# Kernel optimization log

Measured on AMD Instinct MI355X. Metric: run time of the kernel, lower is better.

Reference implementation:

```python
import jax, jax.numpy as jnp
import numpy as np

B, N, C = 8, 2_000_000, 16


def _per_batch_loss(x, t, num_classes):
    """x: [N] float values, t: [N] int labels.
    For each label group: loss = mean(group) - mode(group) (scipy mode,
    ties -> smallest value), scattered back to every position of that label.
    """
    n = x.shape[0]
    # Sort primarily by label, secondarily by value (lexsort: last key primary).
    order = jnp.lexsort((x, t))
    xs = x[order]
    ts = t[order]
    # Run-length encode equal (label, value) pairs to count value multiplicity.
    new_run = jnp.concatenate(
        [jnp.ones((1,), bool), (ts[1:] != ts[:-1]) | (xs[1:] != xs[:-1])])
    run_id = jnp.cumsum(new_run) - 1                      # [N]
    run_cnt = jax.ops.segment_sum(jnp.ones(n, xs.dtype), run_id,
                                  num_segments=n)[run_id]  # count per element
    # Mode per label = smallest value attaining the max multiplicity.
    grp_max = jax.ops.segment_max(run_cnt, ts, num_segments=num_classes)
    mode = jax.ops.segment_min(
        jnp.where(run_cnt == grp_max[ts], xs, jnp.inf), ts,
        num_segments=num_classes)                         # [C]
    ssum = jax.ops.segment_sum(xs, ts, num_segments=num_classes)
    scnt = jax.ops.segment_sum(jnp.ones(n, xs.dtype), ts,
                               num_segments=num_classes)
    mean = ssum / jnp.maximum(scnt, 1.0)
    per_label = jnp.where(scnt > 0, mean - mode, 0.0)     # [C]
    return per_label[t]                                    # scatter back, [N]


def setup_inputs() -> dict:
    key = jax.random.key(0)
    k1, k2 = jax.random.split(key)
    inputs = jax.random.normal(k1, (B, N), dtype=jnp.float32)
    targets = jax.random.randint(k2, (B, N), 0, C, dtype=jnp.int32)
    return {"inputs": inputs, "targets": targets, "num_classes": C}


def reference(inputs, targets, num_classes):
    per_pos = jax.vmap(lambda x, t: _per_batch_loss(x, t, num_classes))(
        inputs, targets)                                   # [B, N]
    return jnp.mean(per_pos)
```

## Files before the change

kernel.cpp:

```cpp
#include <hip/hip_runtime.h>
#include <stdint.h>

#define NUM_C 16
#define NUM_B 8
#define RANGES 64
#define NBKT (NUM_C * RANGES)
#define CHUNK_S 8192
#define TAB 4096
#define MODE_CAP 3072
#define MAX_NB 8

__device__ __forceinline__ unsigned hash_u32(unsigned h) {
    h ^= h >> 16; h *= 0x85ebca6bu;
    h ^= h >> 13; h *= 0xc2b2ae35u;
    h ^= h >> 16;
    return h;
}
__device__ __forceinline__ unsigned canon_key(float v) {
    unsigned k = __float_as_uint(v);
    return (k == 0x80000000u) ? 0u : k;
}
__device__ __forceinline__ unsigned bucket_of(unsigned key, int c) {
    return ((unsigned)c << 6) | (hash_u32(key) >> 26);
}

__global__ void __launch_bounds__(512)
sort_kernel(const float* __restrict__ x, const int* __restrict__ t,
            long long N, int bbase, int nchunk,
            unsigned* __restrict__ keysout, unsigned short* __restrict__ offs)
{
    __shared__ unsigned hist[NBKT];
    __shared__ unsigned lout[CHUNK_S];
    const int lb = blockIdx.x / nchunk;
    const int ch = blockIdx.x % nchunk;
    const int b  = bbase + lb;
    const long long base = (long long)ch * CHUNK_S;
    const int count = (int)((N - base < CHUNK_S) ? (N - base) : CHUNK_S);
    const float* xb = x + (size_t)b * N + base;
    const int*   tb = t + (size_t)b * N + base;
    const int tid = threadIdx.x;

    for (int i = tid; i < NBKT; i += 512) hist[i] = 0u;
    __syncthreads();

    unsigned keys[16], pk[16];
    const int n4 = count >> 2;
    #pragma unroll
    for (int r = 0; r < 4; ++r) {
        const int idx4 = tid + r * 512;
        if (idx4 < n4) {
            float4 v  = ((const float4*)xb)[idx4];
            int4   cc = ((const int4*)tb)[idx4];
            unsigned k0 = canon_key(v.x), b0 = bucket_of(k0, cc.x);
            unsigned k1 = canon_key(v.y), b1 = bucket_of(k1, cc.y);
            unsigned k2 = canon_key(v.z), b2 = bucket_of(k2, cc.z);
            unsigned k3 = canon_key(v.w), b3 = bucket_of(k3, cc.w);
            unsigned p0 = atomicAdd(&hist[b0], 1u);
            unsigned p1 = atomicAdd(&hist[b1], 1u);
            unsigned p2 = atomicAdd(&hist[b2], 1u);
            unsigned p3 = atomicAdd(&hist[b3], 1u);
            keys[r*4+0] = k0; pk[r*4+0] = (b0 << 13) | p0;
            keys[r*4+1] = k1; pk[r*4+1] = (b1 << 13) | p1;
            keys[r*4+2] = k2; pk[r*4+2] = (b2 << 13) | p2;
            keys[r*4+3] = k3; pk[r*4+3] = (b3 << 13) | p3;
        }
    }
    unsigned kex = 0u, pkx = 0u; int hex = 0;
    {
        const int remi = (n4 << 2) + tid;
        if (remi < count) {
            unsigned k = canon_key(xb[remi]);
            unsigned bk = bucket_of(k, tb[remi]);
            unsigned p = atomicAdd(&hist[bk], 1u);
            kex = k; pkx = (bk << 13) | p; hex = 1;
        }
    }
    __syncthreads();

    for (int st = 1; st < NBKT; st <<= 1) {
        const int k0 = tid, k1 = tid + 512;
        unsigned v0 = hist[k0] + ((k0 >= st) ? hist[k0 - st] : 0u);
        unsigned v1 = hist[k1] + ((k1 >= st) ? hist[k1 - st] : 0u);
        __syncthreads();
        hist[k0] = v0; hist[k1] = v1;
        __syncthreads();
    }

    #pragma unroll
    for (int r = 0; r < 4; ++r) {
        const int idx4 = tid + r * 512;
        if (idx4 < n4) {
            #pragma unroll
            for (int c2 = 0; c2 < 4; ++c2) {
                unsigned bk = pk[r*4+c2] >> 13, p = pk[r*4+c2] & 8191u;
                lout[(bk ? hist[bk - 1] : 0u) + p] = keys[r*4+c2];
            }
        }
    }
    if (hex) {
        unsigned bk = pkx >> 13, p = pkx & 8191u;
        lout[(bk ? hist[bk - 1] : 0u) + p] = kex;
    }
    __syncthreads();

    unsigned* kb = keysout + (size_t)lb * N + base;
    if (count == CHUNK_S) {
        #pragma unroll
        for (int r = 0; r < 4; ++r)
            ((uint4*)kb)[tid + r * 512] = ((const uint4*)lout)[tid + r * 512];
    } else {
        for (int i = tid; i < count; i += 512) kb[i] = lout[i];
    }
    unsigned short* orow = offs + ((size_t)lb * nchunk + ch) * 1025;
    orow[tid]       = (unsigned short)(tid ? hist[tid - 1] : 0u);
    orow[tid + 512] = (unsigned short)hist[tid + 511];
    if (tid == 0) orow[1024] = (unsigned short)hist[1023];
}

__global__ void __launch_bounds__(512)
mode_kernel(const unsigned* __restrict__ keysout,
            const unsigned short* __restrict__ offs,
            long long N, int nchunk, int bbase,
            unsigned long long* __restrict__ best,
            double* __restrict__ psum,
            unsigned* __restrict__ pcnt)
{
    __shared__ unsigned keyt[TAB];
    __shared__ unsigned cnt16[TAB / 2];
    __shared__ unsigned staging[MODE_CAP];
    __shared__ unsigned scnt;
    __shared__ unsigned long long redb[8];
    __shared__ double reds[8];

    const unsigned lb = blockIdx.x >> 10;
    const unsigned g  = blockIdx.x & 1023u;
    const unsigned c  = g >> 6;
    const unsigned b  = (unsigned)bbase + lb;
    const int tid = threadIdx.x;

    const uint4 z4 = make_uint4(0u, 0u, 0u, 0u);
    for (int i = tid; i < TAB / 4; i += 512) ((uint4*)keyt)[i] = z4;
    for (int i = tid; i < TAB / 8; i += 512) ((uint4*)cnt16)[i] = z4;
    if (tid == 0) scnt = 0u;
    __syncthreads();

    const unsigned* kb = keysout + (size_t)lb * N;
    const unsigned short* ob = offs + (size_t)lb * nchunk * 1025;

    double ls = 0.0;
    unsigned mo = 0xFFFFFFFFu;

    const int lane = tid & 63, wid = tid >> 6;
    const int sub = lane >> 4, j = lane & 15;
    for (int q = wid * 4 + sub; q < nchunk; q += 32) {
        unsigned s = 0u, len = 0u, pos = 0u;
        if (j == 0) {
            const unsigned short* orow = ob + (size_t)q * 1025;
            s = orow[g];
            len = (unsigned)orow[g + 1] - s;
            pos = atomicAdd(&scnt, len);
        }
        s   = __shfl(s,   sub << 4);
        len = __shfl(len, sub << 4);
        pos = __shfl(pos, sub << 4);
        const unsigned* src = kb + (size_t)q * CHUNK_S + s;
        for (unsigned jj = (unsigned)j; jj < len; jj += 16u) {
            unsigned key = src[jj];
            ls += (double)__uint_as_float(key);
            unsigned o = (key & 0x80000000u) ? ~key : (key | 0x80000000u);
            if (o < mo) mo = o;
            unsigned sp = pos + jj;
            if (sp < MODE_CAP) staging[sp] = o;
        }
    }
    __syncthreads();

    const unsigned n = (scnt < MODE_CAP) ? scnt : MODE_CAP;
    unsigned bc = 0u, bo = 0xFFFFFFFFu;
    for (unsigned base0 = 0; base0 < n; base0 += 2048u) {
        unsigned od[4], h[4], old[4];
        int nv = 0;
        #pragma unroll
        for (int k = 0; k < 4; ++k) {
            unsigned idx = base0 + (unsigned)tid + (unsigned)k * 512u;
            if (idx < n) {
                unsigned o = staging[idx];
                od[k] = o; h[k] = hash_u32(o) & (TAB - 1);
                nv = k + 1;
            }
        }
        #pragma unroll
        for (int k = 0; k < 4; ++k)
            if (k < nv) old[k] = atomicCAS(&keyt[h[k]], 0u, od[k]);
        #pragma unroll
        for (int k = 0; k < 4; ++k) {
            if (k >= nv) continue;
            unsigned o = old[k], hh = h[k];
            const unsigned oo = od[k];
            unsigned cnt = 1u;
            while (o != 0u) {
                if (o == oo) {
                    unsigned sh = (hh & 1u) << 4;
                    unsigned ret = atomicAdd(&cnt16[hh >> 1], 1u << sh);
                    cnt = ((ret >> sh) & 0xFFFFu) + 2u;
                    break;
                }
                hh = (hh + 1u) & (TAB - 1u);
                o = atomicCAS(&keyt[hh], 0u, oo);
            }
            if (cnt >= 2u && (cnt > bc || (cnt == bc && oo < bo))) {
                bc = cnt; bo = oo;
            }
        }
    }

    unsigned long long lbst = bc ? (((unsigned long long)bc << 32)
                                    | (unsigned long long)(~bo)) : 0ull;
    {
        unsigned long long s1 = (1ull << 32) | (unsigned long long)(~mo);
        if (s1 > lbst) lbst = s1;
    }
    #pragma unroll
    for (int sh = 32; sh > 0; sh >>= 1) {
        unsigned long long obv = __shfl_down(lbst, sh);
        if (obv > lbst) lbst = obv;
        ls += __shfl_down(ls, sh);
    }
    if ((tid & 63) == 0) { redb[wid] = lbst; reds[wid] = ls; }
    __syncthreads();
    if (tid == 0) {
        unsigned long long bb = 0ull; double ss = 0.0;
        #pragma unroll
        for (int i = 0; i < 8; ++i) {
            if (redb[i] > bb) bb = redb[i];
            ss += reds[i];
        }
        psum[b * NBKT + g] = ss;
        pcnt[b * NBKT + g] = scnt;
        if (bb) atomicMax(&best[b * NUM_C + c], bb);
    }
}

__global__ void __launch_bounds__(128)
finalize_kernel(const double* __restrict__ psum,
                const unsigned* __restrict__ pcnt,
                const unsigned long long* __restrict__ best,
                float* __restrict__ out, double inv_total)
{
    __shared__ double acc[NUM_B * NUM_C];
    const int i = threadIdx.x;
    const int b = i >> 4, c = i & 15;

    double s = 0.0;
    unsigned long long cnt = 0ull;
    const double*   ps = psum + (size_t)b * NBKT + ((size_t)c << 6);
    const unsigned* pc = pcnt + (size_t)b * NBKT + ((size_t)c << 6);
    for (int r = 0; r < 64; ++r) { s += ps[r]; cnt += pc[r]; }

    double term = 0.0;
    if (cnt > 0ull) {
        unsigned long long p = best[i];
        unsigned ord = 0xFFFFFFFFu - (unsigned)(p & 0xFFFFFFFFull);
        unsigned ub  = (ord & 0x80000000u) ? (ord ^ 0x80000000u) : ~ord;
        float mode = __uint_as_float(ub);
        term = s - (double)cnt * (double)mode;
    }
    acc[i] = term;
    __syncthreads();
    for (int st = 64; st > 0; st >>= 1) {
        if (i < st) acc[i] += acc[i + st];
        __syncthreads();
    }
    if (i == 0) out[0] = (float)(acc[0] * inv_total);
}

extern "C" void kernel_launch(void* const* d_in, const int* in_sizes, int n_in,
                              void* d_out, int out_size, void* d_ws, size_t ws_size,
                              hipStream_t stream)
{
    const float* x = (const float*)d_in[0];
    const int*   t = (const int*)d_in[1];

    const long long total = in_sizes[0];
    const long long N = total / NUM_B;
    const int nchunk = (int)((N + CHUNK_S - 1) / CHUNK_S);

    char* ws = (char*)d_ws;
    size_t off = 0;
    unsigned long long* best = (unsigned long long*)(ws + off);
    off += (size_t)NUM_B * NUM_C * 8;
    double* psum = (double*)(ws + off);
    off += (size_t)NUM_B * NBKT * 8;
    unsigned* pcnt = (unsigned*)(ws + off);
    off += (size_t)NUM_B * NBKT * 4;
    off = (off + 255) & ~(size_t)255;

    const size_t keys_per_b = (size_t)N * 4;
    const size_t offs_per_b = (size_t)nchunk * 1025 * 2;
    const size_t per_b = keys_per_b + offs_per_b + 512;
    size_t remaining = ws_size - off;
    int nb = (int)(remaining / per_b);
    if (nb < 1) nb = 1;
    if (nb > MAX_NB) nb = MAX_NB;
    {
        int rounds = (NUM_B + nb - 1) / nb;
        nb = (NUM_B + rounds - 1) / rounds;
    }

    unsigned* keysout = (unsigned*)(ws + off);
    off += (size_t)nb * keys_per_b;
    off = (off + 255) & ~(size_t)255;
    unsigned short* offsA = (unsigned short*)(ws + off);
    off += (size_t)nb * offs_per_b;

    hipMemsetAsync(best, 0, (size_t)NUM_B * NUM_C * 8, stream);
    for (int r = 0; r < NUM_B; r += nb) {
        const int nbr = (NUM_B - r < nb) ? (NUM_B - r) : nb;
        sort_kernel<<<nbr * nchunk, 512, 0, stream>>>(
            x, t, N, r, nchunk, keysout, offsA);
        mode_kernel<<<nbr * NBKT, 512, 0, stream>>>(
            keysout, offsA, N, nchunk, r, best, psum, pcnt);
    }
    finalize_kernel<<<1, 128, 0, stream>>>(
        psum, pcnt, best, (float*)d_out,
        1.0 / ((double)NUM_B * (double)N));
}
```

Measured before the change: 299.4 us.

## Transpose chunk offsets and process four hash buckets per mode workgroup

```diff
diff --git a/kernel.cpp b/kernel.cpp
--- a/kernel.cpp
+++ b/kernel.cpp
@@ -3,8 +3,8 @@
 
 #define NUM_C 16
 #define NUM_B 8
-#define RANGES 64
-#define NBKT (NUM_C * RANGES)
+#define NBKT (NUM_C * 64)
+#define NGRP 256
 #define CHUNK_S 8192
 #define TAB 4096
 #define MODE_CAP 3072
@@ -26,11 +26,12 @@
 
 __global__ void __launch_bounds__(512)
 sort_kernel(const float* __restrict__ x, const int* __restrict__ t,
-            long long N, int bbase, int nchunk,
-            unsigned* __restrict__ keysout, unsigned short* __restrict__ offs)
+            long long N, int bbase, int nchunk, int nchpad,
+            unsigned* __restrict__ keysout, unsigned short* __restrict__ offsT)
 {
     __shared__ unsigned hist[NBKT];
     __shared__ unsigned lout[CHUNK_S];
+    __shared__ unsigned wsum[8];
     const int lb = blockIdx.x / nchunk;
     const int ch = blockIdx.x % nchunk;
     const int b  = bbase + lb;
@@ -77,12 +78,22 @@
     }
     __syncthreads();
 
-    for (int st = 1; st < NBKT; st <<= 1) {
-        const int k0 = tid, k1 = tid + 512;
-        unsigned v0 = hist[k0] + ((k0 >= st) ? hist[k0 - st] : 0u);
-        unsigned v1 = hist[k1] + ((k1 >= st) ? hist[k1 - st] : 0u);
+    {
+        unsigned b0v = hist[2 * tid], b1v = hist[2 * tid + 1];
+        unsigned s = b0v + b1v, inc = s;
+        const int lane = tid & 63;
+        #pragma unroll
+        for (int d = 1; d < 64; d <<= 1) {
+            unsigned tt = __shfl_up(inc, d);
+            if (lane >= d) inc += tt;
+        }
+        if (lane == 63) wsum[tid >> 6] = inc;
         __syncthreads();
-        hist[k0] = v0; hist[k1] = v1;
+        unsigned wbase = 0;
+        for (int i = 0; i < (tid >> 6); ++i) wbase += wsum[i];
+        unsigned excl = wbase + inc - s;
+        hist[2 * tid]     = excl + b0v;
+        hist[2 * tid + 1] = excl + s;
         __syncthreads();
     }
 
@@ -111,106 +122,150 @@
     } else {
         for (int i = tid; i < count; i += 512) kb[i] = lout[i];
     }
-    unsigned short* orow = offs + ((size_t)lb * nchunk + ch) * 1025;
-    orow[tid]       = (unsigned short)(tid ? hist[tid - 1] : 0u);
-    orow[tid + 512] = (unsigned short)hist[tid + 511];
-    if (tid == 0) orow[1024] = (unsigned short)hist[1023];
+    unsigned short* ocol = offsT + (size_t)lb * 1025 * nchpad + ch;
+    ocol[(size_t)tid * nchpad] = (unsigned short)(tid ? hist[tid - 1] : 0u);
+    ocol[(size_t)(tid + 512) * nchpad] = (unsigned short)hist[tid + 511];
+    if (tid == 0) ocol[(size_t)1024 * nchpad] = (unsigned short)hist[1023];
 }
 
 __global__ void __launch_bounds__(512)
 mode_kernel(const unsigned* __restrict__ keysout,
-            const unsigned short* __restrict__ offs,
-            long long N, int nchunk, int bbase,
+            const unsigned short* __restrict__ offsT,
+            long long N, int nchunk, int nchpad, int bbase,
             unsigned long long* __restrict__ best,
             double* __restrict__ psum,
             unsigned* __restrict__ pcnt)
 {
     __shared__ unsigned keyt[TAB];
     __shared__ unsigned cnt16[TAB / 2];
-    __shared__ unsigned staging[MODE_CAP];
-    __shared__ unsigned scnt;
+    __shared__ unsigned staging[4][MODE_CAP];
+    __shared__ unsigned short rowbuf[5][256];
+    __shared__ unsigned short pos[4][256];
+    __shared__ unsigned tot[4];
     __shared__ unsigned long long redb[8];
     __shared__ double reds[8];
 
-    const unsigned lb = blockIdx.x >> 10;
-    const unsigned g  = blockIdx.x & 1023u;
-    const unsigned c  = g >> 6;
+    const unsigned nwg = gridDim.x;
+    const unsigned logical = (blockIdx.x & 7u) * (nwg >> 3) + (blockIdx.x >> 3);
+    const unsigned lb = logical >> 8;
+    const unsigned G  = logical & 255u;
+    const unsigned g0 = G << 2;
+    const unsigned c  = G >> 4;
     const unsigned b  = (unsigned)bbase + lb;
     const int tid = threadIdx.x;
+    const int lane = tid & 63, wid = tid >> 6;
 
     const uint4 z4 = make_uint4(0u, 0u, 0u, 0u);
     for (int i = tid; i < TAB / 4; i += 512) ((uint4*)keyt)[i] = z4;
     for (int i = tid; i < TAB / 8; i += 512) ((uint4*)cnt16)[i] = z4;
-    if (tid == 0) scnt = 0u;
+
+    const unsigned short* obT = offsT + (size_t)lb * 1025 * nchpad;
+    for (int i = tid; i < 5 * 256; i += 512) {
+        int r = i >> 8, q = i & 255;
+        rowbuf[r][q] = (q < nchunk)
+            ? obT[(size_t)(g0 + r) * nchpad + q] : (unsigned short)0;
+    }
+    __syncthreads();
+
+    if (wid < 4) {
+        const int sb = wid;
+        unsigned lpre[4], run = 0;
+        #pragma unroll
+        for (int k = 0; k < 4; ++k) {
+            int q = lane * 4 + k;
+            lpre[k] = run;
+            run += (unsigned)rowbuf[sb + 1][q] - (unsigned)rowbuf[sb][q];
+        }
+        unsigned inc = run;
+        #pragma unroll
+        for (int d = 1; d < 64; d <<= 1) {
+            unsigned tt = __shfl_up(inc, d);
+            if (lane >= d) inc += tt;
+        }
+        unsigned basex = inc - run;
+        #pragma unroll
+        for (int k = 0; k < 4; ++k)
+            pos[sb][lane * 4 + k] = (unsigned short)(basex + lpre[k]);
+        if (lane == 63) tot[sb] = inc;
+    }
     __syncthreads();
 
     const unsigned* kb = keysout + (size_t)lb * N;
-    const unsigned short* ob = offs + (size_t)lb * nchunk * 1025;
-
     double ls = 0.0;
     unsigned mo = 0xFFFFFFFFu;
 
-    const int lane = tid & 63, wid = tid >> 6;
     const int sub = lane >> 4, j = lane & 15;
-    for (int q = wid * 4 + sub; q < nchunk; q += 32) {
-        unsigned s = 0u, len = 0u, pos = 0u;
-        if (j == 0) {
-            const unsigned short* orow = ob + (size_t)q * 1025;
-            s = orow[g];
-            len = (unsigned)orow[g + 1] - s;
-            pos = atomicAdd(&scnt, len);
-        }
-        s   = __shfl(s,   sub << 4);
-        len = __shfl(len, sub << 4);
-        pos = __shfl(pos, sub << 4);
-        const unsigned* src = kb + (size_t)q * CHUNK_S + s;
-        for (unsigned jj = (unsigned)j; jj < len; jj += 16u) {
-            unsigned key = src[jj];
-            ls += (double)__uint_as_float(key);
-            unsigned o = (key & 0x80000000u) ? ~key : (key | 0x80000000u);
-            if (o < mo) mo = o;
-            unsigned sp = pos + jj;
-            if (sp < MODE_CAP) staging[sp] = o;
-        }
-    }
-    __syncthreads();
-
-    const unsigned n = (scnt < MODE_CAP) ? scnt : MODE_CAP;
+    const int nit = (nchunk + 31) >> 5;
+    for (int it = 0; it < nit; ++it) {
+        int q = it * 32 + wid * 4 + sub;
+        if (q < nchunk) {
+            unsigned s0 = rowbuf[0][q];
+            unsigned rb1 = (unsigned)rowbuf[1][q] - s0;
+            unsigned rb2 = (unsigned)rowbuf[2][q] - s0;
+            unsigned rb3 = (unsigned)rowbuf[3][q] - s0;
+            unsigned len = (unsigned)rowbuf[4][q] - s0;
+            const unsigned* src = kb + (size_t)q * CHUNK_S + s0;
+            for (unsigned jj = (unsigned)j; jj < len; jj += 16u) {
+                unsigned key = src[jj];
+                ls += (double)__uint_as_float(key);
+                unsigned o = (key & 0x80000000u) ? ~key : (key | 0x80000000u);
+                if (o < mo) mo = o;
+                int sb = (jj >= rb2) ? ((jj >= rb3) ? 3 : 2)
+                                     : ((jj >= rb1) ? 1 : 0);
+                unsigned rel = jj - (sb == 0 ? 0u : (sb == 1 ? rb1
+                                    : (sb == 2 ? rb2 : rb3)));
+                unsigned dst = (unsigned)pos[sb][q] + rel;
+                if (dst < MODE_CAP) staging[sb][dst] = o;
+            }
+        }
+    }
+    __syncthreads();
+
     unsigned bc = 0u, bo = 0xFFFFFFFFu;
-    for (unsigned base0 = 0; base0 < n; base0 += 2048u) {
-        unsigned od[4], h[4], old[4];
-        int nv = 0;
-        #pragma unroll
-        for (int k = 0; k < 4; ++k) {
-            unsigned idx = base0 + (unsigned)tid + (unsigned)k * 512u;
-            if (idx < n) {
-                unsigned o = staging[idx];
-                od[k] = o; h[k] = hash_u32(o) & (TAB - 1);
-                nv = k + 1;
+    for (int sb = 0; sb < 4; ++sb) {
+        unsigned n = tot[sb]; if (n > MODE_CAP) n = MODE_CAP;
+        const unsigned* stg = staging[sb];
+        for (unsigned base0 = 0; base0 < n; base0 += 2048u) {
+            unsigned od[4], h[4], old[4];
+            int nv = 0;
+            #pragma unroll
+            for (int k = 0; k < 4; ++k) {
+                unsigned idx = base0 + (unsigned)tid + (unsigned)k * 512u;
+                if (idx < n) {
+                    unsigned o = stg[idx];
+                    od[k] = o; h[k] = hash_u32(o) & (TAB - 1);
+                    nv = k + 1;
+                }
             }
-        }
-        #pragma unroll
-        for (int k = 0; k < 4; ++k)
-            if (k < nv) old[k] = atomicCAS(&keyt[h[k]], 0u, od[k]);
-        #pragma unroll
-        for (int k = 0; k < 4; ++k) {
-            if (k >= nv) continue;
-            unsigned o = old[k], hh = h[k];
-            const unsigned oo = od[k];
-            unsigned cnt = 1u;
-            while (o != 0u) {
-                if (o == oo) {
-                    unsigned sh = (hh & 1u) << 4;
-                    unsigned ret = atomicAdd(&cnt16[hh >> 1], 1u << sh);
-                    cnt = ((ret >> sh) & 0xFFFFu) + 2u;
-                    break;
+            #pragma unroll
+            for (int k = 0; k < 4; ++k)
+                if (k < nv) old[k] = atomicCAS(&keyt[h[k]], 0u, od[k]);
+            #pragma unroll
+            for (int k = 0; k < 4; ++k) {
+                if (k >= nv) continue;
+                unsigned o = old[k], hh = h[k];
+                const unsigned oo = od[k];
+                unsigned cnt = 1u;
+                while (o != 0u) {
+                    if (o == oo) {
+                        unsigned sh = (hh & 1u) << 4;
+                        unsigned ret = atomicAdd(&cnt16[hh >> 1], 1u << sh);
+                        cnt = ((ret >> sh) & 0xFFFFu) + 2u;
+                        break;
+                    }
+                    hh = (hh + 1u) & (TAB - 1u);
+                    o = atomicCAS(&keyt[hh], 0u, oo);
                 }
-                hh = (hh + 1u) & (TAB - 1u);
-                o = atomicCAS(&keyt[hh], 0u, oo);
+                if (cnt >= 2u && (cnt > bc || (cnt == bc && oo < bo))) {
+                    bc = cnt; bo = oo;
+                }
             }
-            if (cnt >= 2u && (cnt > bc || (cnt == bc && oo < bo))) {
-                bc = cnt; bo = oo;
-            }
+        }
+        if (sb < 3) {
+            __syncthreads();
+            for (int i = tid; i < TAB / 4; i += 512) ((uint4*)keyt)[i] = z4;
+            for (int i = tid; i < TAB / 8; i += 512) ((uint4*)cnt16)[i] = z4;
+            __syncthreads();
         }
     }
 
@@ -226,7 +281,7 @@
         if (obv > lbst) lbst = obv;
         ls += __shfl_down(ls, sh);
     }
-    if ((tid & 63) == 0) { redb[wid] = lbst; reds[wid] = ls; }
+    if (lane == 0) { redb[wid] = lbst; reds[wid] = ls; }
     __syncthreads();
     if (tid == 0) {
         unsigned long long bb = 0ull; double ss = 0.0;
@@ -235,8 +290,8 @@
             if (redb[i] > bb) bb = redb[i];
             ss += reds[i];
         }
-        psum[b * NBKT + g] = ss;
-        pcnt[b * NBKT + g] = scnt;
+        psum[b * NGRP + G] = ss;
+        pcnt[b * NGRP + G] = tot[0] + tot[1] + tot[2] + tot[3];
         if (bb) atomicMax(&best[b * NUM_C + c], bb);
     }
 }
@@ -253,9 +308,9 @@
 
     double s = 0.0;
     unsigned long long cnt = 0ull;
-    const double*   ps = psum + (size_t)b * NBKT + ((size_t)c << 6);
-    const unsigned* pc = pcnt + (size_t)b * NBKT + ((size_t)c << 6);
-    for (int r = 0; r < 64; ++r) { s += ps[r]; cnt += pc[r]; }
+    const double*   ps = psum + (size_t)b * NGRP + ((size_t)c << 4);
+    const unsigned* pc = pcnt + (size_t)b * NGRP + ((size_t)c << 4);
+    for (int r = 0; r < 16; ++r) { s += ps[r]; cnt += pc[r]; }
 
     double term = 0.0;
     if (cnt > 0ull) {
@@ -284,19 +339,20 @@
     const long long total = in_sizes[0];
     const long long N = total / NUM_B;
     const int nchunk = (int)((N + CHUNK_S - 1) / CHUNK_S);
+    const int nchpad = (nchunk + 63) & ~63;
 
     char* ws = (char*)d_ws;
     size_t off = 0;
     unsigned long long* best = (unsigned long long*)(ws + off);
     off += (size_t)NUM_B * NUM_C * 8;
     double* psum = (double*)(ws + off);
-    off += (size_t)NUM_B * NBKT * 8;
+    off += (size_t)NUM_B * NGRP * 8;
     unsigned* pcnt = (unsigned*)(ws + off);
-    off += (size_t)NUM_B * NBKT * 4;
+    off += (size_t)NUM_B * NGRP * 4;
     off = (off + 255) & ~(size_t)255;
 
     const size_t keys_per_b = (size_t)N * 4;
-    const size_t offs_per_b = (size_t)nchunk * 1025 * 2;
+    const size_t offs_per_b = (size_t)1025 * nchpad * 2;
     const size_t per_b = keys_per_b + offs_per_b + 512;
     size_t remaining = ws_size - off;
     int nb = (int)(remaining / per_b);
@@ -310,16 +366,16 @@
     unsigned* keysout = (unsigned*)(ws + off);
     off += (size_t)nb * keys_per_b;
     off = (off + 255) & ~(size_t)255;
-    unsigned short* offsA = (unsigned short*)(ws + off);
+    unsigned short* offsT = (unsigned short*)(ws + off);
     off += (size_t)nb * offs_per_b;
 
     hipMemsetAsync(best, 0, (size_t)NUM_B * NUM_C * 8, stream);
     for (int r = 0; r < NUM_B; r += nb) {
         const int nbr = (NUM_B - r < nb) ? (NUM_B - r) : nb;
         sort_kernel<<<nbr * nchunk, 512, 0, stream>>>(
-            x, t, N, r, nchunk, keysout, offsA);
-        mode_kernel<<<nbr * NBKT, 512, 0, stream>>>(
-            keysout, offsA, N, nchunk, r, best, psum, pcnt);
+            x, t, N, r, nchunk, nchpad, keysout, offsT);
+        mode_kernel<<<nbr * NGRP, 512, 0, stream>>>(
+            keysout, offsT, N, nchunk, nchpad, r, best, psum, pcnt);
     }
     finalize_kernel<<<1, 128, 0, stream>>>(
         psum, pcnt, best, (float*)d_out,
```

After: 299.6 us. About the same (+0.1%).

## Replace per-chunk local sort with global hist/scan/place partition into 512 buckets

Applied to the files above, without the earlier changes.

```diff
diff --git a/kernel.cpp b/kernel.cpp
--- a/kernel.cpp
+++ b/kernel.cpp
@@ -3,11 +3,9 @@
 
 #define NUM_C 16
 #define NUM_B 8
-#define RANGES 64
-#define NBKT (NUM_C * RANGES)
+#define NPAIR 512
 #define CHUNK_S 8192
-#define TAB 4096
-#define MODE_CAP 3072
+#define TAB 8192
 #define MAX_NB 8
 
 __device__ __forceinline__ unsigned hash_u32(unsigned h) {
@@ -20,17 +18,16 @@
     unsigned k = __float_as_uint(v);
     return (k == 0x80000000u) ? 0u : k;
 }
-__device__ __forceinline__ unsigned bucket_of(unsigned key, int c) {
-    return ((unsigned)c << 6) | (hash_u32(key) >> 26);
-}
-
-__global__ void __launch_bounds__(512)
-sort_kernel(const float* __restrict__ x, const int* __restrict__ t,
+__device__ __forceinline__ unsigned pair_of(unsigned key, int c) {
+    return ((unsigned)c << 5) | (hash_u32(key) >> 27);
+}
+
+__global__ void __launch_bounds__(512)
+hist_kernel(const float* __restrict__ x, const int* __restrict__ t,
             long long N, int bbase, int nchunk,
-            unsigned* __restrict__ keysout, unsigned short* __restrict__ offs)
-{
-    __shared__ unsigned hist[NBKT];
-    __shared__ unsigned lout[CHUNK_S];
+            unsigned short* __restrict__ counts, unsigned char* __restrict__ t8)
+{
+    __shared__ unsigned hist[NPAIR];
     const int lb = blockIdx.x / nchunk;
     const int ch = blockIdx.x % nchunk;
     const int b  = bbase + lb;
@@ -38,165 +35,211 @@
     const int count = (int)((N - base < CHUNK_S) ? (N - base) : CHUNK_S);
     const float* xb = x + (size_t)b * N + base;
     const int*   tb = t + (size_t)b * N + base;
+    unsigned char* t8b = t8 + (size_t)lb * N + base;
     const int tid = threadIdx.x;
 
-    for (int i = tid; i < NBKT; i += 512) hist[i] = 0u;
-    __syncthreads();
-
-    unsigned keys[16], pk[16];
-    const int n4 = count >> 2;
+    hist[tid] = 0u;
+    __syncthreads();
+
+    const bool vec_ok = ((N & 3) == 0);
+    const int n4 = vec_ok ? (count >> 2) : 0;
     #pragma unroll
     for (int r = 0; r < 4; ++r) {
-        const int idx4 = tid + r * 512;
-        if (idx4 < n4) {
-            float4 v  = ((const float4*)xb)[idx4];
-            int4   cc = ((const int4*)tb)[idx4];
-            unsigned k0 = canon_key(v.x), b0 = bucket_of(k0, cc.x);
-            unsigned k1 = canon_key(v.y), b1 = bucket_of(k1, cc.y);
-            unsigned k2 = canon_key(v.z), b2 = bucket_of(k2, cc.z);
-            unsigned k3 = canon_key(v.w), b3 = bucket_of(k3, cc.w);
-            unsigned p0 = atomicAdd(&hist[b0], 1u);
-            unsigned p1 = atomicAdd(&hist[b1], 1u);
-            unsigned p2 = atomicAdd(&hist[b2], 1u);
-            unsigned p3 = atomicAdd(&hist[b3], 1u);
-            keys[r*4+0] = k0; pk[r*4+0] = (b0 << 13) | p0;
-            keys[r*4+1] = k1; pk[r*4+1] = (b1 << 13) | p1;
-            keys[r*4+2] = k2; pk[r*4+2] = (b2 << 13) | p2;
-            keys[r*4+3] = k3; pk[r*4+3] = (b3 << 13) | p3;
-        }
-    }
-    unsigned kex = 0u, pkx = 0u; int hex = 0;
-    {
-        const int remi = (n4 << 2) + tid;
-        if (remi < count) {
-            unsigned k = canon_key(xb[remi]);
-            unsigned bk = bucket_of(k, tb[remi]);
-            unsigned p = atomicAdd(&hist[bk], 1u);
-            kex = k; pkx = (bk << 13) | p; hex = 1;
-        }
-    }
-    __syncthreads();
-
-    for (int st = 1; st < NBKT; st <<= 1) {
-        const int k0 = tid, k1 = tid + 512;
-        unsigned v0 = hist[k0] + ((k0 >= st) ? hist[k0 - st] : 0u);
-        unsigned v1 = hist[k1] + ((k1 >= st) ? hist[k1 - st] : 0u);
-        __syncthreads();
-        hist[k0] = v0; hist[k1] = v1;
-        __syncthreads();
-    }
-
+        const int i = tid + r * 512;
+        if (i < n4) {
+            float4 v  = ((const float4*)xb)[i];
+            int4   cc = ((const int4*)tb)[i];
+            atomicAdd(&hist[pair_of(canon_key(v.x), cc.x)], 1u);
+            atomicAdd(&hist[pair_of(canon_key(v.y), cc.y)], 1u);
+            atomicAdd(&hist[pair_of(canon_key(v.z), cc.z)], 1u);
+            atomicAdd(&hist[pair_of(canon_key(v.w), cc.w)], 1u);
+            uchar4 q;
+            q.x = (unsigned char)cc.x; q.y = (unsigned char)cc.y;
+            q.z = (unsigned char)cc.z; q.w = (unsigned char)cc.w;
+            ((uchar4*)t8b)[i] = q;
+        }
+    }
+    for (int i = (n4 << 2) + tid; i < count; i += 512) {
+        int c = tb[i];
+        atomicAdd(&hist[pair_of(canon_key(xb[i]), c)], 1u);
+        t8b[i] = (unsigned char)c;
+    }
+    __syncthreads();
+    counts[((size_t)lb * nchunk + ch) * NPAIR + tid] = (unsigned short)hist[tid];
+}
+
+__global__ void __launch_bounds__(512)
+scan_kernel(const unsigned short* __restrict__ counts,
+            unsigned* __restrict__ gpos, unsigned* __restrict__ ptot,
+            int nchunk)
+{
+    __shared__ unsigned short tile[256][32];
+    __shared__ unsigned part[16][32];
+    const int lb = blockIdx.x >> 4;
+    const int c0 = (blockIdx.x & 15) * 32;
+    const int tid = threadIdx.x;
+    const unsigned short* cb = counts + (size_t)lb * nchunk * NPAIR;
+
+    for (int i = tid; i < 256 * 32; i += 512) {
+        int r = i >> 5, cc = i & 31;
+        tile[r][cc] = (r < nchunk)
+            ? cb[(size_t)r * NPAIR + c0 + cc] : (unsigned short)0;
+    }
+    __syncthreads();
+
+    const int col = tid & 31, seg = tid >> 5;
+    unsigned ssum = 0;
+    #pragma unroll
+    for (int r = 0; r < 16; ++r) ssum += tile[seg * 16 + r][col];
+    part[seg][col] = ssum;
+    __syncthreads();
+    if (seg == 0) {
+        unsigned run = 0;
+        #pragma unroll
+        for (int j = 0; j < 16; ++j) {
+            unsigned v = part[j][col]; part[j][col] = run; run += v;
+        }
+        ptot[(size_t)lb * NPAIR + c0 + col] = run;
+    }
+    __syncthreads();
+    unsigned run = part[seg][col];
+    unsigned* gp = gpos + (size_t)lb * nchunk * NPAIR;
+    #pragma unroll
+    for (int r = 0; r < 16; ++r) {
+        int rr = seg * 16 + r;
+        if (rr < nchunk) gp[(size_t)rr * NPAIR + c0 + col] = run;
+        run += tile[rr][col];
+    }
+}
+
+__global__ void __launch_bounds__(512)
+base_kernel(const unsigned* __restrict__ ptot, unsigned* __restrict__ pbase)
+{
+    __shared__ unsigned wsum[8];
+    const int lb = blockIdx.x, tid = threadIdx.x, lane = tid & 63;
+    unsigned v = ptot[(size_t)lb * NPAIR + tid];
+    unsigned inc = v;
+    #pragma unroll
+    for (int d = 1; d < 64; d <<= 1) {
+        unsigned tt = __shfl_up(inc, d);
+        if (lane >= d) inc += tt;
+    }
+    if (lane == 63) wsum[tid >> 6] = inc;
+    __syncthreads();
+    unsigned wbase = 0;
+    for (int i = 0; i < (tid >> 6); ++i) wbase += wsum[i];
+    unsigned excl = wbase + inc - v;
+    unsigned* pb = pbase + (size_t)lb * (NPAIR + 1);
+    pb[tid] = excl;
+    if (tid == NPAIR - 1) pb[NPAIR] = excl + v;
+}
+
+__global__ void __launch_bounds__(512)
+place_kernel(const float* __restrict__ x, const unsigned char* __restrict__ t8,
+             long long N, int bbase, int nchunk,
+             const unsigned* __restrict__ gpos, const unsigned* __restrict__ pbase,
+             unsigned* __restrict__ keysout)
+{
+    __shared__ unsigned off[NPAIR];
+    const int lb = blockIdx.x / nchunk;
+    const int ch = blockIdx.x % nchunk;
+    const int b  = bbase + lb;
+    const long long base = (long long)ch * CHUNK_S;
+    const int count = (int)((N - base < CHUNK_S) ? (N - base) : CHUNK_S);
+    const float* xb = x + (size_t)b * N + base;
+    const unsigned char* t8b = t8 + (size_t)lb * N + base;
+    const int tid = threadIdx.x;
+
+    off[tid] = pbase[(size_t)lb * (NPAIR + 1) + tid]
+             + gpos[((size_t)lb * nchunk + ch) * NPAIR + tid];
+    __syncthreads();
+
+    unsigned* kb = keysout + (size_t)lb * N;
+    const bool vec_ok = ((N & 3) == 0);
+    const int n4 = vec_ok ? (count >> 2) : 0;
     #pragma unroll
     for (int r = 0; r < 4; ++r) {
-        const int idx4 = tid + r * 512;
-        if (idx4 < n4) {
-            #pragma unroll
-            for (int c2 = 0; c2 < 4; ++c2) {
-                unsigned bk = pk[r*4+c2] >> 13, p = pk[r*4+c2] & 8191u;
-                lout[(bk ? hist[bk - 1] : 0u) + p] = keys[r*4+c2];
-            }
-        }
-    }
-    if (hex) {
-        unsigned bk = pkx >> 13, p = pkx & 8191u;
-        lout[(bk ? hist[bk - 1] : 0u) + p] = kex;
-    }
-    __syncthreads();
-
-    unsigned* kb = keysout + (size_t)lb * N + base;
-    if (count == CHUNK_S) {
-        #pragma unroll
-        for (int r = 0; r < 4; ++r)
-            ((uint4*)kb)[tid + r * 512] = ((const uint4*)lout)[tid + r * 512];
-    } else {
-        for (int i = tid; i < count; i += 512) kb[i] = lout[i];
-    }
-    unsigned short* orow = offs + ((size_t)lb * nchunk + ch) * 1025;
-    orow[tid]       = (unsigned short)(tid ? hist[tid - 1] : 0u);
-    orow[tid + 512] = (unsigned short)hist[tid + 511];
-    if (tid == 0) orow[1024] = (unsigned short)hist[1023];
+        const int i = tid + r * 512;
+        if (i < n4) {
+            float4 v  = ((const float4*)xb)[i];
+            uchar4 cc = ((const uchar4*)t8b)[i];
+            unsigned k0 = canon_key(v.x), k1 = canon_key(v.y);
+            unsigned k2 = canon_key(v.z), k3 = canon_key(v.w);
+            unsigned p0 = atomicAdd(&off[pair_of(k0, cc.x)], 1u);
+            unsigned p1 = atomicAdd(&off[pair_of(k1, cc.y)], 1u);
+            unsigned p2 = atomicAdd(&off[pair_of(k2, cc.z)], 1u);
+            unsigned p3 = atomicAdd(&off[pair_of(k3, cc.w)], 1u);
+            kb[p0] = k0; kb[p1] = k1; kb[p2] = k2; kb[p3] = k3;
+        }
+    }
+    for (int i = (n4 << 2) + tid; i < count; i += 512) {
+        unsigned k = canon_key(xb[i]);
+        unsigned p = atomicAdd(&off[pair_of(k, (int)t8b[i])], 1u);
+        kb[p] = k;
+    }
 }
 
 __global__ void __launch_bounds__(512)
 mode_kernel(const unsigned* __restrict__ keysout,
-            const unsigned short* __restrict__ offs,
-            long long N, int nchunk, int bbase,
+            const unsigned* __restrict__ pbase, long long N, int bbase,
             unsigned long long* __restrict__ best,
             double* __restrict__ psum,
             unsigned* __restrict__ pcnt)
 {
     __shared__ unsigned keyt[TAB];
     __shared__ unsigned cnt16[TAB / 2];
-    __shared__ unsigned staging[MODE_CAP];
-    __shared__ unsigned scnt;
     __shared__ unsigned long long redb[8];
     __shared__ double reds[8];
 
-    const unsigned lb = blockIdx.x >> 10;
-    const unsigned g  = blockIdx.x & 1023u;
-    const unsigned c  = g >> 6;
+    const unsigned lb = blockIdx.x >> 9;
+    const unsigned pr = blockIdx.x & 511u;
+    const unsigned c  = pr >> 5;
     const unsigned b  = (unsigned)bbase + lb;
     const int tid = threadIdx.x;
+    const int lane = tid & 63, wid = tid >> 6;
 
     const uint4 z4 = make_uint4(0u, 0u, 0u, 0u);
     for (int i = tid; i < TAB / 4; i += 512) ((uint4*)keyt)[i] = z4;
     for (int i = tid; i < TAB / 8; i += 512) ((uint4*)cnt16)[i] = z4;
-    if (tid == 0) scnt = 0u;
-    __syncthreads();
-
+    __syncthreads();
+
+    const unsigned* pb = pbase + (size_t)lb * (NPAIR + 1);
+    const unsigned s = pb[pr], e = pb[pr + 1];
     const unsigned* kb = keysout + (size_t)lb * N;
-    const unsigned short* ob = offs + (size_t)lb * nchunk * 1025;
 
     double ls = 0.0;
     unsigned mo = 0xFFFFFFFFu;
-
-    const int lane = tid & 63, wid = tid >> 6;
-    const int sub = lane >> 4, j = lane & 15;
-    for (int q = wid * 4 + sub; q < nchunk; q += 32) {
-        unsigned s = 0u, len = 0u, pos = 0u;
-        if (j == 0) {
-            const unsigned short* orow = ob + (size_t)q * 1025;
-            s = orow[g];
-            len = (unsigned)orow[g + 1] - s;
-            pos = atomicAdd(&scnt, len);
-        }
-        s   = __shfl(s,   sub << 4);
-        len = __shfl(len, sub << 4);
-        pos = __shfl(pos, sub << 4);
-        const unsigned* src = kb + (size_t)q * CHUNK_S + s;
-        for (unsigned jj = (unsigned)j; jj < len; jj += 16u) {
-            unsigned key = src[jj];
-            ls += (double)__uint_as_float(key);
-            unsigned o = (key & 0x80000000u) ? ~key : (key | 0x80000000u);
-            if (o < mo) mo = o;
-            unsigned sp = pos + jj;
-            if (sp < MODE_CAP) staging[sp] = o;
-        }
-    }
-    __syncthreads();
-
-    const unsigned n = (scnt < MODE_CAP) ? scnt : MODE_CAP;
     unsigned bc = 0u, bo = 0xFFFFFFFFu;
-    for (unsigned base0 = 0; base0 < n; base0 += 2048u) {
+
+    for (unsigned j4 = s + (unsigned)tid * 4u; j4 < e; j4 += 2048u) {
+        const int nv = (int)((e - j4 < 4u) ? (e - j4) : 4u);
+        unsigned kk[4];
+        #pragma unroll
+        for (int m = 0; m < 4; ++m)
+            kk[m] = (m < nv) ? kb[j4 + (unsigned)m] : 0u;
         unsigned od[4], h[4], old[4];
-        int nv = 0;
-        #pragma unroll
-        for (int k = 0; k < 4; ++k) {
-            unsigned idx = base0 + (unsigned)tid + (unsigned)k * 512u;
-            if (idx < n) {
-                unsigned o = staging[idx];
-                od[k] = o; h[k] = hash_u32(o) & (TAB - 1);
-                nv = k + 1;
+        int dh[4];
+        #pragma unroll
+        for (int m = 0; m < 4; ++m) {
+            dh[m] = 0;
+            if (m < nv) {
+                unsigned key = kk[m];
+                ls += (double)__uint_as_float(key);
+                unsigned o = (key & 0x80000000u) ? ~key : (key | 0x80000000u);
+                if (o < mo) mo = o;
+                od[m] = o;
+                h[m] = hash_u32(o) & (TAB - 1);
+                dh[m] = (j4 + (unsigned)m - s) < (unsigned)TAB;
             }
         }
         #pragma unroll
-        for (int k = 0; k < 4; ++k)
-            if (k < nv) old[k] = atomicCAS(&keyt[h[k]], 0u, od[k]);
-        #pragma unroll
-        for (int k = 0; k < 4; ++k) {
-            if (k >= nv) continue;
-            unsigned o = old[k], hh = h[k];
-            const unsigned oo = od[k];
+        for (int m = 0; m < 4; ++m)
+            if (dh[m]) old[m] = atomicCAS(&keyt[h[m]], 0u, od[m]);
+        #pragma unroll
+        for (int m = 0; m < 4; ++m) {
+            if (!dh[m]) continue;
+            unsigned o = old[m], hh = h[m];
+            const unsigned oo = od[m];
             unsigned cnt = 1u;
             while (o != 0u) {
                 if (o == oo) {
@@ -226,7 +269,7 @@
         if (obv > lbst) lbst = obv;
         ls += __shfl_down(ls, sh);
     }
-    if ((tid & 63) == 0) { redb[wid] = lbst; reds[wid] = ls; }
+    if (lane == 0) { redb[wid] = lbst; reds[wid] = ls; }
     __syncthreads();
     if (tid == 0) {
         unsigned long long bb = 0ull; double ss = 0.0;
@@ -235,8 +278,8 @@
             if (redb[i] > bb) bb = redb[i];
             ss += reds[i];
         }
-        psum[b * NBKT + g] = ss;
-        pcnt[b * NBKT + g] = scnt;
+        psum[b * NPAIR + pr] = ss;
+        pcnt[b * NPAIR + pr] = e - s;
         if (bb) atomicMax(&best[b * NUM_C + c], bb);
     }
 }
@@ -253,9 +296,9 @@
 
     double s = 0.0;
     unsigned long long cnt = 0ull;
-    const double*   ps = psum + (size_t)b * NBKT + ((size_t)c << 6);
-    const unsigned* pc = pcnt + (size_t)b * NBKT + ((size_t)c << 6);
-    for (int r = 0; r < 64; ++r) { s += ps[r]; cnt += pc[r]; }
+    const double*   ps = psum + (size_t)b * NPAIR + ((size_t)c << 5);
+    const unsigned* pc = pcnt + (size_t)b * NPAIR + ((size_t)c << 5);
+    for (int r = 0; r < 32; ++r) { s += ps[r]; cnt += pc[r]; }
 
     double term = 0.0;
     if (cnt > 0ull) {
@@ -290,14 +333,19 @@
     unsigned long long* best = (unsigned long long*)(ws + off);
     off += (size_t)NUM_B * NUM_C * 8;
     double* psum = (double*)(ws + off);
-    off += (size_t)NUM_B * NBKT * 8;
+    off += (size_t)NUM_B * NPAIR * 8;
     unsigned* pcnt = (unsigned*)(ws + off);
-    off += (size_t)NUM_B * NBKT * 4;
-    off = (off + 255) & ~(size_t)255;
-
-    const size_t keys_per_b = (size_t)N * 4;
-    const size_t offs_per_b = (size_t)nchunk * 1025 * 2;
-    const size_t per_b = keys_per_b + offs_per_b + 512;
+    off += (size_t)NUM_B * NPAIR * 4;
+    off = (off + 255) & ~(size_t)255;
+
+    const size_t keys_per_b  = (size_t)N * 4;
+    const size_t t8_per_b    = (size_t)N;
+    const size_t cnts_per_b  = (size_t)nchunk * NPAIR * 2;
+    const size_t gpos_per_b  = (size_t)nchunk * NPAIR * 4;
+    const size_t ptot_per_b  = (size_t)NPAIR * 4;
+    const size_t pbase_per_b = (size_t)(NPAIR + 1) * 4;
+    const size_t per_b = keys_per_b + t8_per_b + cnts_per_b + gpos_per_b
+                       + ptot_per_b + pbase_per_b + 1024;
     size_t remaining = ws_size - off;
     int nb = (int)(remaining / per_b);
     if (nb < 1) nb = 1;
@@ -310,16 +358,33 @@
     unsigned* keysout = (unsigned*)(ws + off);
     off += (size_t)nb * keys_per_b;
     off = (off + 255) & ~(size_t)255;
-    unsigned short* offsA = (unsigned short*)(ws + off);
-    off += (size_t)nb * offs_per_b;
+    unsigned short* counts = (unsigned short*)(ws + off);
+    off += (size_t)nb * cnts_per_b;
+    off = (off + 255) & ~(size_t)255;
+    unsigned* gpos = (unsigned*)(ws + off);
+    off += (size_t)nb * gpos_per_b;
+    off = (off + 255) & ~(size_t)255;
+    unsigned* ptot = (unsigned*)(ws + off);
+    off += (size_t)nb * ptot_per_b;
+    off = (off + 255) & ~(size_t)255;
+    unsigned* pbase = (unsigned*)(ws + off);
+    off += (size_t)nb * pbase_per_b;
+    off = (off + 255) & ~(size_t)255;
+    unsigned char* t8 = (unsigned char*)(ws + off);
+    off += (size_t)nb * t8_per_b;
 
     hipMemsetAsync(best, 0, (size_t)NUM_B * NUM_C * 8, stream);
     for (int r = 0; r < NUM_B; r += nb) {
         const int nbr = (NUM_B - r < nb) ? (NUM_B - r) : nb;
-        sort_kernel<<<nbr * nchunk, 512, 0, stream>>>(
-            x, t, N, r, nchunk, keysout, offsA);
-        mode_kernel<<<nbr * NBKT, 512, 0, stream>>>(
-            keysout, offsA, N, nchunk, r, best, psum, pcnt);
+        hist_kernel<<<nbr * nchunk, 512, 0, stream>>>(
+            x, t, N, r, nchunk, counts, t8);
+        scan_kernel<<<nbr * 16, 512, 0, stream>>>(
+            counts, gpos, ptot, nchunk);
+        base_kernel<<<nbr, 512, 0, stream>>>(ptot, pbase);
+        place_kernel<<<nbr * nchunk, 512, 0, stream>>>(
+            x, t8, N, r, nchunk, gpos, pbase, keysout);
+        mode_kernel<<<nbr * NPAIR, 512, 0, stream>>>(
+            keysout, pbase, N, r, best, psum, pcnt);
     }
     finalize_kernel<<<1, 128, 0, stream>>>(
         psum, pcnt, best, (float*)d_out,
```

Result: slower. 339.0 us (+13.2%).
